# Kernel optimization log

Measured on AMD Instinct MI355X. Metric: run time of the kernel, lower is better.

Reference implementation:

```python
import jax, jax.numpy as jnp
import numpy as np

N = 100000
E = 1000000
IN_C = 128
HID = 128
HEADS = 4
DH = HID // HEADS
L = 2
RWSE_DIM = 16
WALK_LEN = 16
NPAIRS = 200000
EPS = 1e-5


def setup_inputs() -> dict:
    key = jax.random.key(0)
    ks = jax.random.split(key, 20)
    x = jax.random.normal(ks[0], (N, IN_C), dtype=jnp.float32)
    rw_diag = jax.random.uniform(ks[1], (N, WALK_LEN), dtype=jnp.float32)
    edge_index = jax.random.randint(ks[2], (2, E), 0, N, dtype=jnp.int32)
    src = jax.random.randint(ks[3], (NPAIRS,), 0, N, dtype=jnp.int32)
    dst = jax.random.randint(ks[4], (NPAIRS,), 0, N, dtype=jnp.int32)
    s = 0.05
    W_rwse = jax.random.normal(ks[5], (WALK_LEN, RWSE_DIM), dtype=jnp.float32) * s
    b_rwse = jnp.zeros((RWSE_DIM,), dtype=jnp.float32)
    W_in = jax.random.normal(ks[6], (IN_C + RWSE_DIM, HID), dtype=jnp.float32) * s
    b_in = jnp.zeros((HID,), dtype=jnp.float32)
    Wq = jax.random.normal(ks[7], (L, HID, HID), dtype=jnp.float32) * s
    bq = jnp.zeros((L, HID), dtype=jnp.float32)
    Wk = jax.random.normal(ks[8], (L, HID, HID), dtype=jnp.float32) * s
    bk = jnp.zeros((L, HID), dtype=jnp.float32)
    Wv = jax.random.normal(ks[9], (L, HID, HID), dtype=jnp.float32) * s
    bv = jnp.zeros((L, HID), dtype=jnp.float32)
    Ws = jax.random.normal(ks[10], (L, HID, HID), dtype=jnp.float32) * s
    bs = jnp.zeros((L, HID), dtype=jnp.float32)
    ln_g = jnp.ones((L, HID), dtype=jnp.float32)
    ln_b = jnp.zeros((L, HID), dtype=jnp.float32)
    return {"x": x, "rw_diag": rw_diag, "edge_index": edge_index, "src": src,
            "dst": dst, "W_rwse": W_rwse, "b_rwse": b_rwse, "W_in": W_in,
            "b_in": b_in, "Wq": Wq, "bq": bq, "Wk": Wk, "bk": bk, "Wv": Wv,
            "bv": bv, "Ws": Ws, "bs": bs, "ln_g": ln_g, "ln_b": ln_b}


def reference(x, rw_diag, edge_index, src, dst, W_rwse, b_rwse, W_in, b_in,
              Wq, bq, Wk, bk, Wv, bv, Ws, bs, ln_g, ln_b):
    row = edge_index[0]  # message source j
    col = edge_index[1]  # message target i
    # RWSE projection + input projection
    pe = rw_diag @ W_rwse + b_rwse                      # [N, rwse_dim]
    h = jnp.concatenate([x, pe], axis=-1) @ W_in + b_in  # [N, HID]
    scale = 1.0 / jnp.sqrt(jnp.float32(DH))
    for l in range(L):
        q = (h @ Wq[l] + bq[l]).reshape(N, HEADS, DH)
        k = (h @ Wk[l] + bk[l]).reshape(N, HEADS, DH)
        v = (h @ Wv[l] + bv[l]).reshape(N, HEADS, DH)
        # per-edge attention scores (gather)
        score = jnp.einsum('ehd,ehd->eh', q[col], k[row]) * scale  # [E, H]
        # segment softmax over incoming edges of each target node
        m = jax.ops.segment_max(score, col, num_segments=N)   # [N, H]
        ex = jnp.exp(score - m[col])
        z = jax.ops.segment_sum(ex, col, num_segments=N)      # [N, H]
        alpha = ex / z[col]                                   # [E, H]
        agg = jax.ops.segment_sum(alpha[:, :, None] * v[row], col,
                                  num_segments=N).reshape(N, HID)
        conv = agg + h @ Ws[l] + bs[l]  # root/skip linear (PyG lin_skip)
        # residual + LayerNorm + ReLU
        y = h + conv
        mu = jnp.mean(y, axis=-1, keepdims=True)
        var = jnp.mean(jnp.square(y - mu), axis=-1, keepdims=True)
        h = jax.nn.relu(ln_g[l] * (y - mu) / jnp.sqrt(var + EPS) + ln_b[l])
    logits = jnp.sum(h[src] * h[dst], axis=-1)  # [NPAIRS]
    return jax.nn.sigmoid(logits)
```

## Files before the change

kernel.cpp:

```cpp
#include <hip/hip_runtime.h>
#include <hip/hip_bf16.h>
#include <cstdint>


#define NN      100000
#define EE      1000000
#define RWSEC   16
#define WALKC   16
#define NPAIRSC 200000
#define BSH     9
#define BKT     ((NN + 511) >> BSH)

typedef unsigned int       u32;
typedef unsigned short     u16;
typedef unsigned char      u8;
typedef __attribute__((ext_vector_type(8))) short    short8;
typedef __attribute__((ext_vector_type(4))) float    f32x4;
typedef __attribute__((ext_vector_type(2))) _Float16 h2;

__device__ __forceinline__ float bflo(u32 u){ return __uint_as_float(u << 16); }
__device__ __forceinline__ float bfhi(u32 u){ return __uint_as_float(u & 0xffff0000u); }
__device__ __forceinline__ u16 f2bf(float f){
    u32 u = __float_as_uint(f);
    u += 0x7fffu + ((u >> 16) & 1u);
    return (u16)(u >> 16);
}
__device__ __forceinline__ u32 pack2(float a, float b){
    return (u32)f2bf(a) | ((u32)f2bf(b) << 16);
}

#if defined(__has_builtin)
#if __has_builtin(__builtin_amdgcn_cvt_pk_f32_fp8) && __has_builtin(__builtin_amdgcn_cvt_pk_fp8_f32)
#define HWFP8 1
#endif
#if __has_builtin(__builtin_amdgcn_sdot4)
#define USE_SDOT4 1
#endif
#if __has_builtin(__builtin_amdgcn_cvt_pk_f16_fp8)
#define HWF16FP8 1
#endif
#endif

#ifndef HWFP8
__device__ __forceinline__ float fp8dec1(u32 b){
    u32 s = (b >> 7) & 1u, e = (b >> 3) & 15u, m = b & 7u;
    float mag = e ? __uint_as_float(((e + 120u) << 23) | (m << 20))
                  : (float)m * 0.001953125f;
    return s ? -mag : mag;
}
__device__ __forceinline__ u32 fp8enc1(float f){
    u32 u = __float_as_uint(f); u32 s = (u >> 31) << 7; float a = fabsf(f);
    if (a >= 448.f) return s | 0x7Eu;
    u32 ua = __float_as_uint(a);
    ua += 0x7FFFFu + ((ua >> 20) & 1u);
    int e = (int)(ua >> 23) - 127 + 7;
    if (e <= 0){ int m = (int)rintf(a * 512.f); return s | (u32)m; }
    u32 m = (ua >> 20) & 7u;
    return s | ((u32)e << 3) | m;
}
#endif

__device__ __forceinline__ void fp8x4_dec(u32 w4, float& f0, float& f1, float& f2, float& f3){
#ifdef HWFP8
    auto lo = __builtin_amdgcn_cvt_pk_f32_fp8((int)w4, false);
    auto hi = __builtin_amdgcn_cvt_pk_f32_fp8((int)w4, true);
    f0 = lo[0]; f1 = lo[1]; f2 = hi[0]; f3 = hi[1];
#else
    f0 = fp8dec1(w4 & 255u); f1 = fp8dec1((w4 >> 8) & 255u);
    f2 = fp8dec1((w4 >> 16) & 255u); f3 = fp8dec1(w4 >> 24);
#endif
}
__device__ __forceinline__ u32 fp8x4_enc(float f0, float f1, float f2, float f3){
#ifdef HWFP8
    u32 t = (u32)__builtin_amdgcn_cvt_pk_fp8_f32(f0, f1, 0, false);
    return (u32)__builtin_amdgcn_cvt_pk_fp8_f32(f2, f3, (int)t, true);
#else
    return fp8enc1(f0) | (fp8enc1(f1) << 8) | (fp8enc1(f2) << 16) | (fp8enc1(f3) << 24);
#endif
}
__device__ __forceinline__ void fp8x4_to_h2(u32 w, h2& lo, h2& hi){
#ifdef HWF16FP8
    lo = __builtin_bit_cast(h2, __builtin_amdgcn_cvt_pk_f16_fp8((int)w, false));
    hi = __builtin_bit_cast(h2, __builtin_amdgcn_cvt_pk_f16_fp8((int)w, true));
#else
    float f0, f1, f2, f3;
    fp8x4_dec(w, f0, f1, f2, f3);
    lo = __builtin_bit_cast(h2, __builtin_amdgcn_cvt_pkrtz(f0, f1));
    hi = __builtin_bit_cast(h2, __builtin_amdgcn_cvt_pkrtz(f2, f3));
#endif
}
__device__ __forceinline__ h2 h2shfl_add(h2 a, int m){
    int u = __builtin_bit_cast(int, a);
    int o = __shfl_xor(u, m);
    return a + __builtin_bit_cast(h2, o);
}

#define QSCALE    48.0f
#define DESCALE2  1.10693e-4f

__device__ __forceinline__ int i8q(float f){
    float c = fminf(fmaxf(f * QSCALE, -127.f), 127.f);
    return (int)rintf(c);
}
__device__ __forceinline__ u32 i8x4_enc(float f0, float f1, float f2, float f3){
    return (u32)(i8q(f0) & 255) | ((u32)(i8q(f1) & 255) << 8)
         | ((u32)(i8q(f2) & 255) << 16) | ((u32)(i8q(f3) & 255) << 24);
}
__device__ __forceinline__ float sb(u32 w, int i){
    return (float)(int)(signed char)((w >> (i * 8)) & 255u);
}

__global__ __launch_bounds__(256) void winprep_kernel(const float* __restrict__ Win,
                                                      u16* __restrict__ Winb){
    int t = blockIdx.x * 256 + threadIdx.x;
    if (t >= 8 * 5 * 64) return;
    int lane = t & 63, fi = t >> 6;
    int nt = fi / 5, kk = fi - nt * 5;
    int col = nt * 16 + (lane & 15);
    int k0  = kk * 32 + (lane >> 4) * 8;
    u16* dst = Winb + (size_t)fi * 512 + lane * 8;
    #pragma unroll
    for (int e = 0; e < 8; ++e){
        int k = k0 + e;
        dst[e] = (k < 144) ? f2bf(Win[(size_t)k * 128 + col]) : (u16)0;
    }
}

__global__ __launch_bounds__(256) void inproj_mfma(const float* __restrict__ x,
        const float* __restrict__ rw, const float* __restrict__ Wr,
        const float* __restrict__ br,
        const u16* __restrict__ Winb, const float* __restrict__ bin,
        u16* __restrict__ hb){
    __shared__ u16   hs[64 * 168];
    __shared__ float rws[64 * 16];
    __shared__ u16   ob[64 * 128];
    int tid = threadIdx.x;
    int n0  = blockIdx.x * 64;

    #pragma unroll
    for (int i = 0; i < 32; ++i){
        int g   = i * 256 + tid;
        int row = g >> 5, c4 = g & 31;
        float4 f = make_float4(0.f, 0.f, 0.f, 0.f);
        if (n0 + row < NN)
            f = *reinterpret_cast<const float4*>(x + (size_t)(n0 + row) * 128 + c4 * 4);
        *reinterpret_cast<uint2*>((char*)hs + row * 336 + c4 * 8)
            = make_uint2(pack2(f.x, f.y), pack2(f.z, f.w));
    }
    {
        int row = tid >> 2, c4 = tid & 3;
        float4 f = make_float4(0.f, 0.f, 0.f, 0.f);
        if (n0 + row < NN)
            f = *reinterpret_cast<const float4*>(rw + (size_t)(n0 + row) * 16 + c4 * 4);
        *reinterpret_cast<float4*>(&rws[row * 16 + c4 * 4]) = f;
    }
    __syncthreads();
    {
        int row = tid >> 2, j0 = (tid & 3) * 4;
        float p0 = br[j0], p1 = br[j0 + 1], p2 = br[j0 + 2], p3 = br[j0 + 3];
        #pragma unroll
        for (int w = 0; w < 16; ++w){
            float r = rws[row * 16 + w];
            const float4 wv = *reinterpret_cast<const float4*>(Wr + w * 16 + j0);
            p0 = fmaf(r, wv.x, p0); p1 = fmaf(r, wv.y, p1);
            p2 = fmaf(r, wv.z, p2); p3 = fmaf(r, wv.w, p3);
        }
        *reinterpret_cast<uint2*>((char*)hs + row * 336 + 256 + (tid & 3) * 8)
            = make_uint2(pack2(p0, p1), pack2(p2, p3));
        *reinterpret_cast<uint2*>((char*)hs + row * 336 + 288 + (tid & 3) * 8)
            = make_uint2(0u, 0u);
    }
    __syncthreads();

    int l = tid & 63, w = tid >> 6;
    int r16 = l & 15, kq = l >> 4;
    short8 ha[4][5];
    #pragma unroll
    for (int rg = 0; rg < 4; ++rg)
        #pragma unroll
        for (int kk = 0; kk < 5; ++kk){
            int row = rg * 16 + r16;
            ha[rg][kk] = *reinterpret_cast<const short8*>(
                (const char*)hs + row * 336 + kk * 64 + kq * 16);
        }
    #pragma unroll
    for (int nt2 = 0; nt2 < 2; ++nt2){
        int nt = w * 2 + nt2;
        const short8* wfrag = reinterpret_cast<const short8*>(Winb) + (size_t)(nt * 5) * 64;
        f32x4 acc[4];
        #pragma unroll
        for (int rg = 0; rg < 4; ++rg) acc[rg] = (f32x4){0.f, 0.f, 0.f, 0.f};
        #pragma unroll
        for (int kk = 0; kk < 5; ++kk){
            short8 wf = wfrag[kk * 64 + l];
            #pragma unroll
            for (int rg = 0; rg < 4; ++rg)
                acc[rg] = __builtin_amdgcn_mfma_f32_16x16x32_bf16(wf, ha[rg][kk], acc[rg], 0, 0, 0);
        }
        float4 bvv = *reinterpret_cast<const float4*>(bin + nt * 16 + kq * 4);
        #pragma unroll
        for (int rg = 0; rg < 4; ++rg){
            u32 p0 = pack2(acc[rg][0] + bvv.x, acc[rg][1] + bvv.y);
            u32 p1 = pack2(acc[rg][2] + bvv.z, acc[rg][3] + bvv.w);
            int row = rg * 16 + r16;
            int cb  = (nt * 32 + kq * 8) ^ ((row & 7) << 4);
            *reinterpret_cast<uint2*>((char*)ob + row * 256 + cb) = make_uint2(p0, p1);
        }
    }
    __syncthreads();
    #pragma unroll
    for (int i = 0; i < 4; ++i){
        int row = i * 16 + (tid >> 4);
        int cb  = (tid & 15) * 16;
        uint4 v = *reinterpret_cast<const uint4*>(
            (char*)ob + row * 256 + (cb ^ ((row & 7) << 4)));
        if (n0 + row < NN)
            *reinterpret_cast<uint4*>(hb + (size_t)(n0 + row) * 128 + cb / 2) = v;
    }
}

__global__ __launch_bounds__(256) void bhist_kernel(const int* __restrict__ col,
                                                    int* __restrict__ bcnt){
    __shared__ int h[BKT];
    int tid = threadIdx.x;
    for (int i = tid; i < BKT; i += 256) h[i] = 0;
    __syncthreads();
    for (int e = blockIdx.x * 256 + tid; e < EE; e += gridDim.x * 256)
        atomicAdd(&h[col[e] >> BSH], 1);
    __syncthreads();
    for (int i = tid; i < BKT; i += 256)
        if (h[i]) atomicAdd(&bcnt[i], h[i]);
}

__global__ __launch_bounds__(256) void bscan_kernel(const int* __restrict__ bcnt,
                                                    int* __restrict__ bstart,
                                                    int* __restrict__ bwork){
    __shared__ int lds[256];
    int tid = threadIdx.x;
    int v = (tid < BKT) ? bcnt[tid] : 0;
    lds[tid] = v;
    __syncthreads();
    for (int off = 1; off < 256; off <<= 1){
        int y = (tid >= off) ? lds[tid - off] : 0;
        __syncthreads();
        lds[tid] += y;
        __syncthreads();
    }
    if (tid < BKT){ int p = lds[tid] - v; bstart[tid] = p; bwork[tid] = p; }
}

__global__ __launch_bounds__(256) void bpart_kernel(const int* __restrict__ ei,
                                                    int* __restrict__ bwork,
                                                    u32* __restrict__ bkt){
    __shared__ int cnt_[BKT], base_[BKT], rnk_[BKT];
    int tid = threadIdx.x;
    for (int i = tid; i < BKT; i += 256){ cnt_[i] = 0; rnk_[i] = 0; }
    __syncthreads();
    for (int e = blockIdx.x * 256 + tid; e < EE; e += gridDim.x * 256)
        atomicAdd(&cnt_[ei[EE + e] >> BSH], 1);
    __syncthreads();
    for (int i = tid; i < BKT; i += 256)
        base_[i] = cnt_[i] ? atomicAdd(&bwork[i], cnt_[i]) : 0;
    __syncthreads();
    for (int e = blockIdx.x * 256 + tid; e < EE; e += gridDim.x * 256){
        int c = ei[EE + e], b = c >> BSH;
        int p = base_[b] + atomicAdd(&rnk_[b], 1);
        bkt[p] = ((u32)ei[e] << BSH) | (u32)(c & 511);
    }
}

__global__ __launch_bounds__(256) void bcsr_kernel(const int* __restrict__ bstart,
                                                   const int* __restrict__ bcnt,
                                                   const u32* __restrict__ bkt,
                                                   int* __restrict__ offs,
                                                   int* __restrict__ deg,
                                                   int* __restrict__ ebuf){
    __shared__ int dcnt[512];
    __shared__ int pref[512];
    __shared__ int psum[256];
    int b   = blockIdx.x;
    int tid = threadIdx.x;
    int n0  = b << BSH;
    int nb  = NN - n0 < 512 ? NN - n0 : 512;
    int e0  = bstart[b];
    int ec  = bcnt[b];
    dcnt[tid] = 0; dcnt[tid + 256] = 0;
    __syncthreads();
    for (int i = tid; i < ec; i += 256)
        atomicAdd(&dcnt[bkt[e0 + i] & 511u], 1);
    __syncthreads();
    int s0 = dcnt[2 * tid], s1 = dcnt[2 * tid + 1];
    psum[tid] = s0 + s1;
    __syncthreads();
    for (int off = 1; off < 256; off <<= 1){
        int y = (tid >= off) ? psum[tid - off] : 0;
        __syncthreads();
        psum[tid] += y;
        __syncthreads();
    }
    int exq = psum[tid] - (s0 + s1);
    pref[2 * tid]     = exq;
    pref[2 * tid + 1] = exq + s0;
    __syncthreads();
    for (int i = tid; i < nb; i += 256){
        offs[n0 + i] = e0 + pref[i];
        deg[n0 + i]  = dcnt[i];
    }
    __syncthreads();
    for (int i = tid; i < ec; i += 256){
        u32 rc = bkt[e0 + i];
        int p = atomicAdd(&pref[rc & 511u], 1);
        ebuf[e0 + p] = (int)(rc >> BSH);
    }
}

__global__ __launch_bounds__(256) void wprep_kernel(const float* __restrict__ Wq,
        const float* __restrict__ Wk, const float* __restrict__ Wv,
        const float* __restrict__ Ws, u16* __restrict__ Wb2){
    int t = blockIdx.x * 256 + threadIdx.x;
    if (t >= 2 * 128 * 64) return;
    int lane = t & 63, fi = (t >> 6) & 127, l = t >> 13;
    int gnt = fi >> 2, kk = fi & 3;
    int m = gnt >> 3;
    int col = (gnt * 16 + (lane & 15)) & 127;
    const float* W = (m == 0 ? Wq : m == 1 ? Wk : m == 2 ? Wv : Ws) + (size_t)l * 16384;
    int k0 = kk * 32 + (lane >> 4) * 8;
    u16* dst = Wb2 + ((size_t)l * 128 + fi) * 512 + lane * 8;
    #pragma unroll
    for (int e = 0; e < 8; ++e) dst[e] = f2bf(W[(size_t)(k0 + e) * 128 + col]);
}

__global__ __launch_bounds__(256) void gemm4_mfma(const u16* __restrict__ hb,
        const u16* __restrict__ Wb2,
        const float* __restrict__ bq, const float* __restrict__ bk,
        const float* __restrict__ bv, const float* __restrict__ bs,
        u8* __restrict__ qb, u8* __restrict__ kvb, u16* __restrict__ hsb){
    __shared__ u16 hs[64 * 128];
    __shared__ u16 ob[4][64 * 128];
    int tid = threadIdx.x;
    int n0  = blockIdx.x * 64;
    #pragma unroll
    for (int i = 0; i < 4; ++i){
        int c = i * 256 + tid;
        int row = c >> 4, cb = (c & 15) * 16;
        uint4 v = make_uint4(0u, 0u, 0u, 0u);
        if (n0 + row < NN)
            v = *reinterpret_cast<const uint4*>(hb + (size_t)(n0 + row) * 128 + cb / 2);
        *reinterpret_cast<uint4*>((char*)hs + row * 256 + (cb ^ ((row & 7) << 4))) = v;
    }
    __syncthreads();
    int l = tid & 63, w = tid >> 6;
    int r16 = l & 15, kq = l >> 4;
    short8 ha[4][4];
    #pragma unroll
    for (int rg = 0; rg < 4; ++rg)
        #pragma unroll
        for (int kk = 0; kk < 4; ++kk){
            int row = rg * 16 + r16;
            int byt = (kk * 64 + kq * 16) ^ ((row & 7) << 4);
            ha[rg][kk] = *reinterpret_cast<const short8*>((const char*)hs + row * 256 + byt);
        }
    const float* bp = w == 0 ? bq : w == 1 ? bk : w == 2 ? bv : bs;
    const short8* wfrag = reinterpret_cast<const short8*>(Wb2) + (size_t)(w * 8) * 4 * 64;
    u16* myob = &ob[w][0];
    #pragma unroll
    for (int nt = 0; nt < 8; ++nt){
        f32x4 acc[4];
        #pragma unroll
        for (int rg = 0; rg < 4; ++rg) acc[rg] = (f32x4){0.f, 0.f, 0.f, 0.f};
        #pragma unroll
        for (int kk = 0; kk < 4; ++kk){
            short8 wf = wfrag[(nt * 4 + kk) * 64 + l];
            #pragma unroll
            for (int rg = 0; rg < 4; ++rg)
                acc[rg] = __builtin_amdgcn_mfma_f32_16x16x32_bf16(wf, ha[rg][kk], acc[rg], 0, 0, 0);
        }
        float4 bvv = *reinterpret_cast<const float4*>(bp + nt * 16 + kq * 4);
        #pragma unroll
        for (int rg = 0; rg < 4; ++rg){
            int row = rg * 16 + r16;
            int cb  = (nt * 32 + kq * 8) ^ ((row & 7) << 4);
            float a0 = acc[rg][0] + bvv.x, a1 = acc[rg][1] + bvv.y;
            float a2 = acc[rg][2] + bvv.z, a3 = acc[rg][3] + bvv.w;
            if (w == 3){
                uint2 hval = *reinterpret_cast<const uint2*>((const char*)hs + row * 256 + cb);
                a0 += bflo(hval.x); a1 += bfhi(hval.x);
                a2 += bflo(hval.y); a3 += bfhi(hval.y);
            }
            *reinterpret_cast<uint2*>((char*)myob + row * 256 + cb)
                = make_uint2(pack2(a0, a1), pack2(a2, a3));
        }
    }
    asm volatile("s_waitcnt lgkmcnt(0)" ::: "memory");
    if (w == 1 || w == 2){
        int off = (w == 2) ? 8 : 0;
        #pragma unroll
        for (int i = 0; i < 16; ++i){
            int row = i * 4 + kq;
            int cb  = r16 * 16;
            uint4 v = *reinterpret_cast<const uint4*>(
                (char*)myob + row * 256 + (cb ^ ((row & 7) << 4)));
            if (n0 + row < NN){
                u32 A, B;
#ifdef USE_SDOT4
                if (w == 1){
                    A = i8x4_enc(bflo(v.x), bfhi(v.x), bflo(v.y), bfhi(v.y));
                    B = i8x4_enc(bflo(v.z), bfhi(v.z), bflo(v.w), bfhi(v.w));
                } else
#endif
                {
                    A = fp8x4_enc(bflo(v.x), bfhi(v.x), bflo(v.y), bfhi(v.y));
                    B = fp8x4_enc(bflo(v.z), bfhi(v.z), bflo(v.w), bfhi(v.w));
                }
                *reinterpret_cast<uint2*>((char*)kvb + (size_t)(n0 + row) * 256
                                          + r16 * 16 + off) = make_uint2(A, B);
            }
        }
    } else if (w == 0){
        #pragma unroll
        for (int i = 0; i < 16; ++i){
            int row = i * 4 + kq;
            int cb  = r16 * 16;
            uint4 v = *reinterpret_cast<const uint4*>(
                (char*)myob + row * 256 + (cb ^ ((row & 7) << 4)));
            if (n0 + row < NN){
#ifdef USE_SDOT4
                u32 A = i8x4_enc(bflo(v.x), bfhi(v.x), bflo(v.y), bfhi(v.y));
                u32 B = i8x4_enc(bflo(v.z), bfhi(v.z), bflo(v.w), bfhi(v.w));
                *reinterpret_cast<uint2*>(qb + (size_t)(n0 + row) * 128 + cb / 2)
                    = make_uint2(A, B);
#else
                *reinterpret_cast<uint4*>((u16*)qb + (size_t)(n0 + row) * 128 + cb / 2) = v;
#endif
            }
        }
    } else {
        #pragma unroll
        for (int i = 0; i < 16; ++i){
            int row = i * 4 + kq;
            int cb  = r16 * 16;
            uint4 v = *reinterpret_cast<const uint4*>(
                (char*)myob + row * 256 + (cb ^ ((row & 7) << 4)));
            if (n0 + row < NN)
                *reinterpret_cast<uint4*>(hsb + (size_t)(n0 + row) * 128 + cb / 2) = v;
        }
    }
}

__global__ __launch_bounds__(256) void attn_kernel(u16* __restrict__ hb,
        const u8* __restrict__ qb, const u8* __restrict__ kvb,
        const u16* __restrict__ hsb,
        const int* __restrict__ offs, const int* __restrict__ deg,
        const int* __restrict__ ebuf,
        const float* __restrict__ gw, const float* __restrict__ bta){
    int tid  = threadIdx.x;
    int lane = tid & 63;
    int n    = blockIdx.x * 4 + (tid >> 6);
    int eq = lane >> 4, gq = lane & 15;
#ifdef USE_SDOT4
    uint2 qu = *reinterpret_cast<const uint2*>(qb + (size_t)n * 128 + gq * 8);
    int qi0 = (int)qu.x, qi1 = (int)qu.y;
#else
    const float scale = 0.17677669529663687f;
    uint4 qu = *reinterpret_cast<const uint4*>((const u16*)qb + (size_t)n * 128 + gq * 8);
    float q0 = bflo(qu.x) * scale, q1 = bfhi(qu.x) * scale;
    float q2 = bflo(qu.y) * scale, q3 = bfhi(qu.y) * scale;
    float q4 = bflo(qu.z) * scale, q5 = bfhi(qu.z) * scale;
    float q6 = bflo(qu.w) * scale, q7 = bfhi(qu.w) * scale;
#endif
    int beg = offs[n], cnt = deg[n];
    float z = 0.f;
    h2 acc01 = (h2)0, acc23 = (h2)0, acc45 = (h2)0, acc67 = (h2)0;

#ifdef USE_SDOT4
    #define SCORE(kv)                                                                 \
        float s;                                                                      \
        {   int si = __builtin_amdgcn_sdot4((int)kv.x, qi0, 0, false);                \
            si = __builtin_amdgcn_sdot4((int)kv.y, qi1, si, false);                   \
            s = (float)si * DESCALE2; }
#else
    #define SCORE(kv)                                                                 \
        float s;                                                                      \
        {   s = q0*sb(kv.x,0) + q1*sb(kv.x,1) + q2*sb(kv.x,2) + q3*sb(kv.x,3)         \
              + q4*sb(kv.y,0) + q5*sb(kv.y,1) + q6*sb(kv.y,2) + q7*sb(kv.y,3);        \
            s *= (1.4426950408889634f / QSCALE); }
#endif

    #define EDGE4(r_, ok_)                                                            \
    {   uint4 kv = *reinterpret_cast<const uint4*>(kvb + (size_t)(r_) * 256 + gq * 16); \
        SCORE(kv);                                                                    \
        s += __shfl_xor(s, 1); s += __shfl_xor(s, 2);                                 \
        float ex = (ok_) ? exp2f(s) : 0.f;                                            \
        h2 v01, v23, v45, v67;                                                        \
        fp8x4_to_h2(kv.z, v01, v23);                                                  \
        fp8x4_to_h2(kv.w, v45, v67);                                                  \
        z += ex;                                                                      \
        _Float16 exh = (_Float16)ex;                                                  \
        h2 exv = {exh, exh};                                                          \
        acc01 = __builtin_elementwise_fma(exv, v01, acc01);                           \
        acc23 = __builtin_elementwise_fma(exv, v23, acc23);                           \
        acc45 = __builtin_elementwise_fma(exv, v45, acc45);                           \
        acc67 = __builtin_elementwise_fma(exv, v67, acc67);  }

    int t = 0;
    for (; t + 8 <= cnt; t += 8){
        int ra = ebuf[beg + t + eq];
        int rb = ebuf[beg + t + 4 + eq];
        EDGE4(ra, true);
        EDGE4(rb, true);
    }
    if (t + 4 <= cnt){
        int ra = ebuf[beg + t + eq];
        EDGE4(ra, true);
        t += 4;
    }
    if (t < cnt){
        int idx = t + eq;
        int r = ebuf[beg + (idx < cnt ? idx : cnt - 1)];
        EDGE4(r, idx < cnt);
    }
    #undef EDGE4
    #undef SCORE

    z += __shfl_xor(z, 16);  z += __shfl_xor(z, 32);
    acc01 = h2shfl_add(acc01, 16); acc01 = h2shfl_add(acc01, 32);
    acc23 = h2shfl_add(acc23, 16); acc23 = h2shfl_add(acc23, 32);
    acc45 = h2shfl_add(acc45, 16); acc45 = h2shfl_add(acc45, 32);
    acc67 = h2shfl_add(acc67, 16); acc67 = h2shfl_add(acc67, 32);
    float rz = (cnt > 0) ? 1.f / z : 0.f;
    float a0 = (float)acc01[0], a1 = (float)acc01[1];
    float a2 = (float)acc23[0], a3 = (float)acc23[1];
    float a4 = (float)acc45[0], a5 = (float)acc45[1];
    float a6 = (float)acc67[0], a7 = (float)acc67[1];

    size_t p = (size_t)n * 128 + gq * 8;
    uint4 hu = *reinterpret_cast<const uint4*>(hsb + p);
    float y0 = bflo(hu.x) + a0 * rz, y1 = bfhi(hu.x) + a1 * rz;
    float y2 = bflo(hu.y) + a2 * rz, y3 = bfhi(hu.y) + a3 * rz;
    float y4 = bflo(hu.z) + a4 * rz, y5 = bfhi(hu.z) + a5 * rz;
    float y6 = bflo(hu.w) + a6 * rz, y7 = bfhi(hu.w) + a7 * rz;
    float sum = y0 + y1 + y2 + y3 + y4 + y5 + y6 + y7;
    float sq  = y0*y0 + y1*y1 + y2*y2 + y3*y3 + y4*y4 + y5*y5 + y6*y6 + y7*y7;
    #pragma unroll
    for (int m = 1; m < 16; m <<= 1){
        sum += __shfl_xor(sum, m);
        sq  += __shfl_xor(sq,  m);
    }
    float mu  = sum * (1.f / 128.f);
    float var = sq * (1.f / 128.f) - mu * mu;
    var = var < 0.f ? 0.f : var;
    float inv = rsqrtf(var + 1e-5f);
    int c = gq * 8;
    float4 gm0 = *reinterpret_cast<const float4*>(gw + c);
    float4 gm1 = *reinterpret_cast<const float4*>(gw + c + 4);
    float4 bt0 = *reinterpret_cast<const float4*>(bta + c);
    float4 bt1 = *reinterpret_cast<const float4*>(bta + c + 4);
    float o0 = fmaf(gm0.x * (y0 - mu), inv, bt0.x);
    float o1 = fmaf(gm0.y * (y1 - mu), inv, bt0.y);
    float o2 = fmaf(gm0.z * (y2 - mu), inv, bt0.z);
    float o3 = fmaf(gm0.w * (y3 - mu), inv, bt0.w);
    float o4 = fmaf(gm1.x * (y4 - mu), inv, bt1.x);
    float o5 = fmaf(gm1.y * (y5 - mu), inv, bt1.y);
    float o6 = fmaf(gm1.z * (y6 - mu), inv, bt1.z);
    float o7 = fmaf(gm1.w * (y7 - mu), inv, bt1.w);
    o0 = o0 > 0.f ? o0 : 0.f;  o1 = o1 > 0.f ? o1 : 0.f;
    o2 = o2 > 0.f ? o2 : 0.f;  o3 = o3 > 0.f ? o3 : 0.f;
    o4 = o4 > 0.f ? o4 : 0.f;  o5 = o5 > 0.f ? o5 : 0.f;
    o6 = o6 > 0.f ? o6 : 0.f;  o7 = o7 > 0.f ? o7 : 0.f;
    if (eq == 0)
        *reinterpret_cast<uint4*>(hb + p) = make_uint4(
            pack2(o0, o1), pack2(o2, o3), pack2(o4, o5), pack2(o6, o7));
}

__global__ __launch_bounds__(256) void pair_kernel(const u16* __restrict__ hb,
                                                   const int* __restrict__ src,
                                                   const int* __restrict__ dst,
                                                   float* __restrict__ out){
    int tid = threadIdx.x;
    int pid = blockIdx.x * 16 + (tid >> 4);
    int sub = tid & 15;
    int s = src[pid], d = dst[pid];
    uint4 a = *reinterpret_cast<const uint4*>(hb + (size_t)s * 128 + sub * 8);
    uint4 b = *reinterpret_cast<const uint4*>(hb + (size_t)d * 128 + sub * 8);
    float dot = bflo(a.x) * bflo(b.x) + bfhi(a.x) * bfhi(b.x)
              + bflo(a.y) * bflo(b.y) + bfhi(a.y) * bfhi(b.y)
              + bflo(a.z) * bflo(b.z) + bfhi(a.z) * bfhi(b.z)
              + bflo(a.w) * bflo(b.w) + bfhi(a.w) * bfhi(b.w);
    dot += __shfl_xor(dot, 1); dot += __shfl_xor(dot, 2);
    dot += __shfl_xor(dot, 4); dot += __shfl_xor(dot, 8);
    if (sub == 0) out[pid] = 1.f / (1.f + __expf(-dot));
}

extern "C" void kernel_launch(void* const* d_in, const int* in_sizes, int n_in,
                              void* d_out, int out_size, void* d_ws, size_t ws_size,
                              hipStream_t stream){
    const float* x      = (const float*)d_in[0];
    const float* rw     = (const float*)d_in[1];
    const int*   ei     = (const int*)  d_in[2];
    const int*   src    = (const int*)  d_in[3];
    const int*   dst    = (const int*)  d_in[4];
    const float* W_rwse = (const float*)d_in[5];
    const float* b_rwse = (const float*)d_in[6];
    const float* W_in   = (const float*)d_in[7];
    const float* b_in   = (const float*)d_in[8];
    const float* Wq     = (const float*)d_in[9];
    const float* bq     = (const float*)d_in[10];
    const float* Wk     = (const float*)d_in[11];
    const float* bk     = (const float*)d_in[12];
    const float* Wv     = (const float*)d_in[13];
    const float* bv     = (const float*)d_in[14];
    const float* Wsk    = (const float*)d_in[15];
    const float* bsk    = (const float*)d_in[16];
    const float* ln_g   = (const float*)d_in[17];
    const float* ln_b   = (const float*)d_in[18];
    float* out = (float*)d_out;

    char* p = (char*)d_ws;
    auto carve = [&](size_t bytes) -> char* {
        char* r = p; p += (bytes + 255) & ~(size_t)255; return r;
    };
    u16*   hb    = (u16*) carve((size_t)NN * 128 * 2);
    u8*    qb    = (u8*)  carve((size_t)NN * 128 * 2);
    u8*    kvb   = (u8*)  carve((size_t)NN * 256);
    u16*   hsb   = (u16*) carve((size_t)NN * 128 * 2);
    int*   offs  = (int*) carve((size_t)NN * 4);
    int*   deg   = (int*) carve((size_t)NN * 4);
    int*   ebuf  = (int*) carve((size_t)EE * 4);
    u32*   bkt   = (u32*) carve((size_t)EE * 4);
    int*   bcnt  = (int*) carve((size_t)BKT * 4);
    int*   bstart= (int*) carve((size_t)BKT * 4);
    int*   bwork = (int*) carve((size_t)BKT * 4);
    u16*   Wb2   = (u16*) carve((size_t)2 * 128 * 512 * 2);
    u16*   Winb  = (u16*) carve((size_t)8 * 5 * 512 * 2);

    hipMemsetAsync(bcnt, 0, (size_t)BKT * 4, stream);

    winprep_kernel<<<10, 256, 0, stream>>>(W_in, Winb);
    wprep_kernel<<<64, 256, 0, stream>>>(Wq, Wk, Wv, Wsk, Wb2);
    inproj_mfma<<<(NN + 63) / 64, 256, 0, stream>>>(x, rw, W_rwse, b_rwse,
                                                    Winb, b_in, hb);
    bhist_kernel<<<512, 256, 0, stream>>>(ei + EE, bcnt);
    bscan_kernel<<<1, 256, 0, stream>>>(bcnt, bstart, bwork);
    bpart_kernel<<<512, 256, 0, stream>>>(ei, bwork, bkt);
    bcsr_kernel<<<BKT, 256, 0, stream>>>(bstart, bcnt, bkt, offs, deg, ebuf);

    for (int l = 0; l < 2; ++l){
        gemm4_mfma<<<(NN + 63) / 64, 256, 0, stream>>>(hb, Wb2 + (size_t)l * 65536,
            bq + l * 128, bk + l * 128, bv + l * 128, bsk + l * 128,
            qb, kvb, hsb);
        attn_kernel<<<NN / 4, 256, 0, stream>>>(hb, qb, kvb, hsb,
            offs, deg, ebuf, ln_g + l * 128, ln_b + l * 128);
    }
    pair_kernel<<<NPAIRSC / 16, 256, 0, stream>>>(hb, src, dst, out);
}
```

Before: 334.2 us.

## Map one node per 16-lane group, sorted by degree, with prefetched edge gathers

The attention kernel now gives each target node a 16-lane group, so 16 nodes share a block, instead of splitting a node's edges over four 16-lane subgroups of a wavefront. Nodes are reordered by in-degree with new histogram, scan and fill kernels, which keeps the groups in a wavefront on similar edge counts. The edge buffer stores pre-shifted byte offsets, and the next K/V row is loaded before the current one is consumed. This removes the cross-subgroup shuffle reductions and the tail masking. In exchange there are three extra setup kernels, edge loads within a node are serial with less memory parallelism per node, and the store order by permuted node is scattered.

```diff
diff --git a/kernel.cpp b/kernel.cpp
--- a/kernel.cpp
+++ b/kernel.cpp
@@ -88,11 +88,6 @@
     lo = __builtin_bit_cast(h2, __builtin_amdgcn_cvt_pkrtz(f0, f1));
     hi = __builtin_bit_cast(h2, __builtin_amdgcn_cvt_pkrtz(f2, f3));
 #endif
-}
-__device__ __forceinline__ h2 h2shfl_add(h2 a, int m){
-    int u = __builtin_bit_cast(int, a);
-    int o = __shfl_xor(u, m);
-    return a + __builtin_bit_cast(h2, o);
 }
 
 #define QSCALE    48.0f
@@ -310,7 +305,48 @@
     for (int i = tid; i < ec; i += 256){
         u32 rc = bkt[e0 + i];
         int p = atomicAdd(&pref[rc & 511u], 1);
-        ebuf[e0 + p] = (int)(rc >> BSH);
+        ebuf[e0 + p] = (int)((rc >> BSH) << 8);
+    }
+}
+
+__global__ __launch_bounds__(256) void dhist_kernel(const int* __restrict__ deg,
+                                                    int* __restrict__ dh){
+    __shared__ int h[256];
+    int tid = threadIdx.x;
+    h[tid] = 0;
+    __syncthreads();
+    for (int i = blockIdx.x * 256 + tid; i < NN; i += gridDim.x * 256){
+        int d = deg[i]; d = d > 255 ? 255 : d;
+        atomicAdd(&h[d], 1);
+    }
+    __syncthreads();
+    if (h[tid]) atomicAdd(&dh[tid], h[tid]);
+}
+
+__global__ __launch_bounds__(256) void dscan_kernel(const int* __restrict__ dh,
+                                                    int* __restrict__ dcur){
+    __shared__ int lds[256];
+    int tid = threadIdx.x;
+    int v = dh[tid];
+    lds[tid] = v;
+    __syncthreads();
+    for (int off = 1; off < 256; off <<= 1){
+        int y = (tid >= off) ? lds[tid - off] : 0;
+        __syncthreads();
+        lds[tid] += y;
+        __syncthreads();
+    }
+    dcur[tid] = lds[tid] - v;
+}
+
+__global__ __launch_bounds__(256) void dfill_kernel(const int* __restrict__ deg,
+                                                    int* __restrict__ dcur,
+                                                    int* __restrict__ perm){
+    int i = blockIdx.x * 256 + threadIdx.x;
+    if (i < NN){
+        int d = deg[i]; d = d > 255 ? 255 : d;
+        int p = atomicAdd(&dcur[d], 1);
+        perm[p] = i;
     }
 }
 
@@ -451,12 +487,11 @@
         const u8* __restrict__ qb, const u8* __restrict__ kvb,
         const u16* __restrict__ hsb,
         const int* __restrict__ offs, const int* __restrict__ deg,
-        const int* __restrict__ ebuf,
+        const int* __restrict__ ebuf, const int* __restrict__ perm,
         const float* __restrict__ gw, const float* __restrict__ bta){
-    int tid  = threadIdx.x;
-    int lane = tid & 63;
-    int n    = blockIdx.x * 4 + (tid >> 6);
-    int eq = lane >> 4, gq = lane & 15;
+    int tid = threadIdx.x;
+    int gq  = tid & 15;
+    int n   = perm[blockIdx.x * 16 + (tid >> 4)];
 #ifdef USE_SDOT4
     uint2 qu = *reinterpret_cast<const uint2*>(qb + (size_t)n * 128 + gq * 8);
     int qi0 = (int)qu.x, qi1 = (int)qu.y;
@@ -471,6 +506,7 @@
     int beg = offs[n], cnt = deg[n];
     float z = 0.f;
     h2 acc01 = (h2)0, acc23 = (h2)0, acc45 = (h2)0, acc67 = (h2)0;
+    const u8* kvg = kvb + gq * 16;
 
 #ifdef USE_SDOT4
     #define SCORE(kv)                                                                 \
@@ -486,11 +522,10 @@
             s *= (1.4426950408889634f / QSCALE); }
 #endif
 
-    #define EDGE4(r_, ok_)                                                            \
-    {   uint4 kv = *reinterpret_cast<const uint4*>(kvb + (size_t)(r_) * 256 + gq * 16); \
-        SCORE(kv);                                                                    \
+    #define CONSUME(kv)                                                               \
+    {   SCORE(kv);                                                                    \
         s += __shfl_xor(s, 1); s += __shfl_xor(s, 2);                                 \
-        float ex = (ok_) ? exp2f(s) : 0.f;                                            \
+        float ex = exp2f(s);                                                          \
         h2 v01, v23, v45, v67;                                                        \
         fp8x4_to_h2(kv.z, v01, v23);                                                  \
         fp8x4_to_h2(kv.w, v45, v67);                                                  \
@@ -502,31 +537,21 @@
         acc45 = __builtin_elementwise_fma(exv, v45, acc45);                           \
         acc67 = __builtin_elementwise_fma(exv, v67, acc67);  }
 
-    int t = 0;
-    for (; t + 8 <= cnt; t += 8){
-        int ra = ebuf[beg + t + eq];
-        int rb = ebuf[beg + t + 4 + eq];
-        EDGE4(ra, true);
-        EDGE4(rb, true);
-    }
-    if (t + 4 <= cnt){
-        int ra = ebuf[beg + t + eq];
-        EDGE4(ra, true);
-        t += 4;
-    }
-    if (t < cnt){
-        int idx = t + eq;
-        int r = ebuf[beg + (idx < cnt ? idx : cnt - 1)];
-        EDGE4(r, idx < cnt);
-    }
-    #undef EDGE4
+    #define GATHER(off_) (*reinterpret_cast<const uint4*>(kvg + (size_t)(u32)(off_)))
+
+    if (cnt > 0){
+        uint4 kv = GATHER(ebuf[beg]);
+        for (int t = 1; t < cnt; ++t){
+            uint4 nk = GATHER(ebuf[beg + t]);
+            CONSUME(kv);
+            kv = nk;
+        }
+        CONSUME(kv);
+    }
+    #undef CONSUME
+    #undef GATHER
     #undef SCORE
 
-    z += __shfl_xor(z, 16);  z += __shfl_xor(z, 32);
-    acc01 = h2shfl_add(acc01, 16); acc01 = h2shfl_add(acc01, 32);
-    acc23 = h2shfl_add(acc23, 16); acc23 = h2shfl_add(acc23, 32);
-    acc45 = h2shfl_add(acc45, 16); acc45 = h2shfl_add(acc45, 32);
-    acc67 = h2shfl_add(acc67, 16); acc67 = h2shfl_add(acc67, 32);
     float rz = (cnt > 0) ? 1.f / z : 0.f;
     float a0 = (float)acc01[0], a1 = (float)acc01[1];
     float a2 = (float)acc23[0], a3 = (float)acc23[1];
@@ -567,9 +592,8 @@
     o2 = o2 > 0.f ? o2 : 0.f;  o3 = o3 > 0.f ? o3 : 0.f;
     o4 = o4 > 0.f ? o4 : 0.f;  o5 = o5 > 0.f ? o5 : 0.f;
     o6 = o6 > 0.f ? o6 : 0.f;  o7 = o7 > 0.f ? o7 : 0.f;
-    if (eq == 0)
-        *reinterpret_cast<uint4*>(hb + p) = make_uint4(
-            pack2(o0, o1), pack2(o2, o3), pack2(o4, o5), pack2(o6, o7));
+    *reinterpret_cast<uint4*>(hb + p) = make_uint4(
+        pack2(o0, o1), pack2(o2, o3), pack2(o4, o5), pack2(o6, o7));
 }
 
 __global__ __launch_bounds__(256) void pair_kernel(const u16* __restrict__ hb,
@@ -630,10 +654,14 @@
     int*   bcnt  = (int*) carve((size_t)BKT * 4);
     int*   bstart= (int*) carve((size_t)BKT * 4);
     int*   bwork = (int*) carve((size_t)BKT * 4);
+    int*   perm  = (int*) carve((size_t)NN * 4);
+    int*   dh    = (int*) carve((size_t)256 * 4);
+    int*   dcur  = (int*) carve((size_t)256 * 4);
     u16*   Wb2   = (u16*) carve((size_t)2 * 128 * 512 * 2);
     u16*   Winb  = (u16*) carve((size_t)8 * 5 * 512 * 2);
 
     hipMemsetAsync(bcnt, 0, (size_t)BKT * 4, stream);
+    hipMemsetAsync(dh, 0, (size_t)256 * 4, stream);
 
     winprep_kernel<<<10, 256, 0, stream>>>(W_in, Winb);
     wprep_kernel<<<64, 256, 0, stream>>>(Wq, Wk, Wv, Wsk, Wb2);
@@ -643,13 +671,16 @@
     bscan_kernel<<<1, 256, 0, stream>>>(bcnt, bstart, bwork);
     bpart_kernel<<<512, 256, 0, stream>>>(ei, bwork, bkt);
     bcsr_kernel<<<BKT, 256, 0, stream>>>(bstart, bcnt, bkt, offs, deg, ebuf);
+    dhist_kernel<<<256, 256, 0, stream>>>(deg, dh);
+    dscan_kernel<<<1, 256, 0, stream>>>(dh, dcur);
+    dfill_kernel<<<(NN + 255) / 256, 256, 0, stream>>>(deg, dcur, perm);
 
     for (int l = 0; l < 2; ++l){
         gemm4_mfma<<<(NN + 63) / 64, 256, 0, stream>>>(hb, Wb2 + (size_t)l * 65536,
             bq + l * 128, bk + l * 128, bv + l * 128, bsk + l * 128,
             qb, kvb, hsb);
-        attn_kernel<<<NN / 4, 256, 0, stream>>>(hb, qb, kvb, hsb,
-            offs, deg, ebuf, ln_g + l * 128, ln_b + l * 128);
+        attn_kernel<<<NN / 16, 256, 0, stream>>>(hb, qb, kvb, hsb,
+            offs, deg, ebuf, perm, ln_g + l * 128, ln_b + l * 128);
     }
     pair_kernel<<<NPAIRSC / 16, 256, 0, stream>>>(hb, src, dst, out);
 }
```

Result: slower. 648.6 us (+94.1%).
